# Kernel optimization log

Hardware: AMD Instinct MI355X
Metric: run time of the kernel (lower is better)

Reference implementation:

```python
import jax, jax.numpy as jnp
import numpy as np

INF = 1000000000.0
N_HEAD, QK_DIM, V_DIM, D_MODEL = 16, 64, 64, 1024
B, S = 4, 2048


def rope(x):
    # x: [b, s, h, d]; standard rotary embedding over interleaved pairs
    b, s, h, d = x.shape
    inv_freq = 1.0 / (10000.0 ** (jnp.arange(0, d, 2, dtype=jnp.float32) / d))  # [d/2]
    ang = jnp.arange(s, dtype=jnp.float32)[:, None] * inv_freq  # [s, d/2]
    cos = jnp.cos(ang)[None, :, None, :]  # [1, s, 1, d/2]
    sin = jnp.sin(ang)[None, :, None, :]
    x1, x2 = x[..., 0::2], x[..., 1::2]
    out_even = x1 * cos - x2 * sin
    out_odd = x1 * sin + x2 * cos
    return jnp.stack([out_even, out_odd], axis=-1).reshape(x.shape)


def setup_inputs() -> dict:
    key = jax.random.key(0)
    ks = jax.random.split(key, 8)
    q = jax.random.normal(ks[0], (B, S, D_MODEL), dtype=jnp.float32)
    k = jax.random.normal(ks[1], (B, S, D_MODEL), dtype=jnp.float32)
    v = jax.random.normal(ks[2], (B, S, D_MODEL), dtype=jnp.float32)
    sd = 1.0 / np.sqrt(D_MODEL)
    Wq = jax.random.normal(ks[3], (D_MODEL, N_HEAD * QK_DIM), dtype=jnp.float32) * sd
    Wk = jax.random.normal(ks[4], (D_MODEL, N_HEAD * QK_DIM), dtype=jnp.float32) * sd
    Wv = jax.random.normal(ks[5], (D_MODEL, N_HEAD * V_DIM), dtype=jnp.float32) * sd
    Wo = jax.random.normal(ks[6], (N_HEAD * V_DIM, D_MODEL), dtype=jnp.float32) * (1.0 / np.sqrt(N_HEAD * V_DIM))
    mask = jnp.broadcast_to(jnp.tril(jnp.ones((S, S), dtype=jnp.int32)), (B, S, S))  # causal
    return {"q": q, "k": k, "v": v, "Wq": Wq, "Wk": Wk, "Wv": Wv, "Wo": Wo, "mask": mask}


def reference(q, k, v, Wq, Wk, Wv, Wo, mask):
    b, ql, _ = q.shape
    kl = k.shape[1]
    Q = (q @ Wq).reshape(b, ql, N_HEAD, QK_DIM)
    K = (k @ Wk).reshape(b, kl, N_HEAD, QK_DIM)
    V = (v @ Wv).reshape(b, kl, N_HEAD, V_DIM)
    Q, K = rope(Q), rope(K)
    scale = QK_DIM ** 0.5
    # [b, h, q, k]
    attn = jnp.einsum('bqhd,bkhd->bhqk', Q / scale, K)
    attn = jnp.where(mask[:, None, :, :] == 0, -INF, attn)
    attn = jax.nn.softmax(attn, axis=-1)
    out = jnp.einsum('bhqk,bkhd->bqhd', attn, V).reshape(b, ql, N_HEAD * V_DIM)
    return out @ Wo
```

## Files before the change

### kernel.cpp

```cpp
#include <hip/hip_runtime.h>
#include <hip/hip_bf16.h>


typedef __attribute__((ext_vector_type(8))) short bf16x8;
typedef __attribute__((ext_vector_type(4))) float f32x4;

static __device__ __forceinline__ short f2bf(float f) {
    union { float f; unsigned u; } v; v.f = f;
    unsigned r = v.u + 0x7fffu + ((v.u >> 16) & 1u);
    return (short)(r >> 16);
}
static __device__ __forceinline__ float bf2f(short s) {
    union { unsigned u; float f; } v; v.u = ((unsigned)(unsigned short)s) << 16;
    return v.f;
}

static __device__ __forceinline__ void gload_lds16(const short* g, short* l) {
    __builtin_amdgcn_global_load_lds(
        (const __attribute__((address_space(1))) void*)g,
        (__attribute__((address_space(3))) void*)l, 16, 0, 0);
}

__global__ __launch_bounds__(256) void cvt4_k(const float* __restrict__ in,
                                              short* __restrict__ out, int n4) {
    int i = blockIdx.x * 256 + threadIdx.x;
    if (i < n4) {
        float4 v = ((const float4*)in)[i];
        unsigned lo = (unsigned)(unsigned short)f2bf(v.x) |
                      ((unsigned)(unsigned short)f2bf(v.y) << 16);
        unsigned hi = (unsigned)(unsigned short)f2bf(v.z) |
                      ((unsigned)(unsigned short)f2bf(v.w) << 16);
        uint2 p; p.x = lo; p.y = hi;
        ((uint2*)out)[i] = p;
    }
}

__global__ __launch_bounds__(256) void cvtWT_k(const float* __restrict__ in,
                                               short* __restrict__ out) {
    __shared__ short tile[64][65];
    int n0 = blockIdx.x * 64, k0 = blockIdx.y * 64;
    int t = threadIdx.x;
#pragma unroll
    for (int i = 0; i < 16; ++i) {
        int e = t + i * 256; int r = e >> 6, cq = e & 63;
        tile[r][cq] = f2bf(in[(size_t)(k0 + r) * 1024 + n0 + cq]);
    }
    __syncthreads();
#pragma unroll
    for (int i = 0; i < 16; ++i) {
        int e = t + i * 256; int r = e >> 6, cq = e & 63;
        out[(size_t)(n0 + r) * 1024 + k0 + cq] = tile[cq][r];
    }
}

__global__ __launch_bounds__(256) void gemm128(const short* __restrict__ A,
                                               const short* __restrict__ Wt,
                                               void* __restrict__ outv, int mode) {
    __shared__ __align__(16) short As[128 * 32];
    __shared__ __align__(16) short Bs[128 * 32];
    int t = threadIdx.x, w = t >> 6, lane = t & 63, c = lane & 15, g = lane >> 4;
    int m0 = blockIdx.y * 128, n0 = blockIdx.x * 128;
    int wm = (w >> 1) * 64, wn = (w & 1) * 64;
    f32x4 acc[4][4];
#pragma unroll
    for (int i = 0; i < 4; ++i)
#pragma unroll
        for (int j = 0; j < 4; ++j) acc[i][j] = (f32x4){0.f, 0.f, 0.f, 0.f};
    int srow = w * 32 + (lane >> 2);
    int skc  = (lane & 3) * 8;
    const short* Ag0 = A  + (size_t)(m0 + srow) * 1024 + skc;
    const short* Ag1 = Ag0 + (size_t)16 * 1024;
    const short* Bg0 = Wt + (size_t)(n0 + srow) * 1024 + skc;
    const short* Bg1 = Bg0 + (size_t)16 * 1024;
    short* al0 = &As[(w * 32) * 32];
    short* al1 = &As[(w * 32 + 16) * 32];
    short* bl0 = &Bs[(w * 32) * 32];
    short* bl1 = &Bs[(w * 32 + 16) * 32];
    for (int kt = 0; kt < 1024; kt += 32) {
        __syncthreads();
        gload_lds16(Ag0 + kt, al0);
        gload_lds16(Ag1 + kt, al1);
        gload_lds16(Bg0 + kt, bl0);
        gload_lds16(Bg1 + kt, bl1);
        __syncthreads();
        bf16x8 af[4], bfr[4];
#pragma unroll
        for (int mi = 0; mi < 4; ++mi)
            af[mi] = *(const bf16x8*)&As[(wm + mi * 16 + c) * 32 + g * 8];
#pragma unroll
        for (int ni = 0; ni < 4; ++ni)
            bfr[ni] = *(const bf16x8*)&Bs[(wn + ni * 16 + c) * 32 + g * 8];
#pragma unroll
        for (int mi = 0; mi < 4; ++mi)
#pragma unroll
            for (int ni = 0; ni < 4; ++ni)
                acc[mi][ni] = __builtin_amdgcn_mfma_f32_16x16x32_bf16(
                    af[mi], bfr[ni], acc[mi][ni], 0, 0, 0);
    }
#pragma unroll
    for (int mi = 0; mi < 4; ++mi)
#pragma unroll
        for (int ni = 0; ni < 4; ++ni)
#pragma unroll
            for (int r = 0; r < 4; ++r) {
                int row = m0 + wm + mi * 16 + g * 4 + r;
                int col = n0 + wn + ni * 16 + c;
                float val = acc[mi][ni][r];
                if (mode == 0) {
                    int b = row >> 11, s = row & 2047, h = col >> 6, d = col & 63;
                    ((short*)outv)[(((size_t)b * 16 + h) * 2048 + s) * 64 + d] = f2bf(val);
                } else if (mode == 1) {
                    int b = row >> 11, s = row & 2047, h = col >> 6, d = col & 63;
                    ((short*)outv)[(((size_t)b * 16 + h) * 64 + d) * 2048 + s] = f2bf(val);
                } else {
                    if (!(val == val)) val = 0.f;
                    ((float*)outv)[(size_t)row * 1024 + col] = val;
                }
            }
}

__global__ __launch_bounds__(256) void rope_k(short* __restrict__ buf) {
    int idx = blockIdx.x * 256 + threadIdx.x;
    int j = idx & 31; int s = (idx >> 5) & 2047; int bh = idx >> 16;
    size_t off = ((size_t)bh * 2048 + s) * 64 + 2 * j;
    unsigned pr = *(unsigned*)&buf[off];
    float x1 = bf2f((short)(pr & 0xffff));
    float x2 = bf2f((short)(pr >> 16));
    float inv = expf(-(float)j * (9.210340371976184f / 32.0f));
    float ang = (float)s * inv;
    float sn = sinf(ang), cs = cosf(ang);
    float e = x1 * cs - x2 * sn;
    float o = x1 * sn + x2 * cs;
    unsigned op = (unsigned)(unsigned short)f2bf(e) |
                  ((unsigned)(unsigned short)f2bf(o) << 16);
    *(unsigned*)&buf[off] = op;
}

__global__ __launch_bounds__(256) void attn_k(const short* __restrict__ Qb,
                                              const short* __restrict__ Kb,
                                              const short* __restrict__ Vt,
                                              short* __restrict__ ctx) {
    __shared__ __align__(16) short Kl[64 * 72];
    __shared__ __align__(16) short Vl[64 * 72];
    __shared__ __align__(16) short Pl[4 * 16 * 72];
    int bx = blockIdx.x, bh = blockIdx.y;
    int t = threadIdx.x, w = t >> 6, lane = t & 63, c = lane & 15, g = lane >> 4;
    int b = bh >> 4, h = bh & 15;
    const short* Qp = Qb + (size_t)bh * 2048 * 64;
    const short* Kp = Kb + (size_t)bh * 2048 * 64;
    const short* Vp = Vt + (size_t)bh * 64 * 2048;
    short* Pw = Pl + w * 16 * 72;
    int ch0 = t * 2, ch1 = t * 2 + 1;
    int row0 = ch0 >> 3, cc0 = ch0 & 7, row1 = ch1 >> 3, cc1 = ch1 & 7;
    for (int pass = 0; pass < 2; ++pass) {
        int qblk = pass ? (31 - bx) : bx;
        int q0 = qblk * 64;
        int qrow = q0 + w * 16 + c;
        bf16x8 qa0 = *(const bf16x8*)(Qp + (size_t)qrow * 64 + g * 8);
        bf16x8 qa1 = *(const bf16x8*)(Qp + (size_t)qrow * 64 + 32 + g * 8);
        f32x4 oacc[4];
        float m_i[4], l_i[4];
#pragma unroll
        for (int r = 0; r < 4; ++r) {
            oacc[r] = (f32x4){0.f, 0.f, 0.f, 0.f};
            m_i[r] = -1e30f; l_i[r] = 0.f;
        }
        uint4 kv0 = *(const uint4*)(Kp + (size_t)row0 * 64 + cc0 * 8);
        uint4 kv1 = *(const uint4*)(Kp + (size_t)row1 * 64 + cc1 * 8);
        uint4 vv0 = *(const uint4*)(Vp + (size_t)row0 * 2048 + cc0 * 8);
        uint4 vv1 = *(const uint4*)(Vp + (size_t)row1 * 2048 + cc1 * 8);
        for (int kb = 0; kb <= qblk; ++kb) {
            int k0 = kb * 64;
            __syncthreads();
            *(uint4*)&Kl[row0 * 72 + cc0 * 8] = kv0;
            *(uint4*)&Kl[row1 * 72 + cc1 * 8] = kv1;
            *(uint4*)&Vl[row0 * 72 + cc0 * 8] = vv0;
            *(uint4*)&Vl[row1 * 72 + cc1 * 8] = vv1;
            __syncthreads();
            if (kb < qblk) {
                int kn = k0 + 64;
                kv0 = *(const uint4*)(Kp + (size_t)(kn + row0) * 64 + cc0 * 8);
                kv1 = *(const uint4*)(Kp + (size_t)(kn + row1) * 64 + cc1 * 8);
                vv0 = *(const uint4*)(Vp + (size_t)row0 * 2048 + kn + cc0 * 8);
                vv1 = *(const uint4*)(Vp + (size_t)row1 * 2048 + kn + cc1 * 8);
            }
            f32x4 sacc[4];
#pragma unroll
            for (int ns = 0; ns < 4; ++ns) sacc[ns] = (f32x4){0.f, 0.f, 0.f, 0.f};
#pragma unroll
            for (int ns = 0; ns < 4; ++ns) {
                bf16x8 b0 = *(const bf16x8*)&Kl[(ns * 16 + c) * 72 + g * 8];
                bf16x8 b1 = *(const bf16x8*)&Kl[(ns * 16 + c) * 72 + 32 + g * 8];
                sacc[ns] = __builtin_amdgcn_mfma_f32_16x16x32_bf16(qa0, b0, sacc[ns], 0, 0, 0);
                sacc[ns] = __builtin_amdgcn_mfma_f32_16x16x32_bf16(qa1, b1, sacc[ns], 0, 0, 0);
            }
            float sv[4][4], pr[4][4];
#pragma unroll
            for (int ns = 0; ns < 4; ++ns)
#pragma unroll
                for (int r = 0; r < 4; ++r) {
                    float x = sacc[ns][r] * 0.125f;
                    int qi = q0 + w * 16 + g * 4 + r;
                    int kj = k0 + ns * 16 + c;
                    sv[ns][r] = (kj > qi) ? -1e30f : x;
                }
#pragma unroll
            for (int r = 0; r < 4; ++r) {
                float bm = fmaxf(fmaxf(sv[0][r], sv[1][r]), fmaxf(sv[2][r], sv[3][r]));
#pragma unroll
                for (int off = 1; off < 16; off <<= 1) bm = fmaxf(bm, __shfl_xor(bm, off));
                float mn = fmaxf(m_i[r], bm);
                float alpha = __expf(m_i[r] - mn);
                float rs = 0.f;
#pragma unroll
                for (int ns = 0; ns < 4; ++ns) {
                    float p = __expf(sv[ns][r] - mn);
                    pr[ns][r] = p; rs += p;
                }
#pragma unroll
                for (int off = 1; off < 16; off <<= 1) rs += __shfl_xor(rs, off);
                l_i[r] = l_i[r] * alpha + rs;
                m_i[r] = mn;
#pragma unroll
                for (int vs = 0; vs < 4; ++vs) oacc[vs][r] *= alpha;
            }
#pragma unroll
            for (int ns = 0; ns < 4; ++ns)
#pragma unroll
                for (int r = 0; r < 4; ++r)
                    Pw[(g * 4 + r) * 72 + ns * 16 + c] = f2bf(pr[ns][r]);
#pragma unroll
            for (int ks = 0; ks < 2; ++ks) {
                bf16x8 pa = *(const bf16x8*)&Pw[c * 72 + ks * 32 + g * 8];
#pragma unroll
                for (int vs = 0; vs < 4; ++vs) {
                    bf16x8 bv = *(const bf16x8*)&Vl[(vs * 16 + c) * 72 + ks * 32 + g * 8];
                    oacc[vs] = __builtin_amdgcn_mfma_f32_16x16x32_bf16(pa, bv, oacc[vs], 0, 0, 0);
                }
            }
        }
#pragma unroll
        for (int vs = 0; vs < 4; ++vs)
#pragma unroll
            for (int r = 0; r < 4; ++r) {
                float val = oacc[vs][r] / l_i[r];
                int qi = q0 + w * 16 + g * 4 + r;
                ctx[((size_t)b * 2048 + qi) * 1024 + h * 64 + vs * 16 + c] = f2bf(val);
            }
    }
}

extern "C" void kernel_launch(void* const* d_in, const int* in_sizes, int n_in,
                              void* d_out, int out_size, void* d_ws, size_t ws_size,
                              hipStream_t stream) {
    const float* q  = (const float*)d_in[0];
    const float* k  = (const float*)d_in[1];
    const float* v  = (const float*)d_in[2];
    const float* Wq = (const float*)d_in[3];
    const float* Wk = (const float*)d_in[4];
    const float* Wv = (const float*)d_in[5];
    const float* Wo = (const float*)d_in[6];
    char* sc = (char*)d_in[7];
    const size_t MB = 1024 * 1024;
    short* qb16 = (short*)(sc + 0 * MB);
    short* kb16 = (short*)(sc + 16 * MB);
    short* vb16 = (short*)(sc + 32 * MB);
    short* WqT  = (short*)(sc + 48 * MB);
    short* WkT  = (short*)(sc + 50 * MB);
    short* WvT  = (short*)(sc + 52 * MB);
    short* WoT  = (short*)(sc + 54 * MB);
    short* qbuf = (short*)d_in[0];
    short* kbuf = (short*)d_in[1];
    short* vtb  = (short*)d_in[2];
    short* ctx  = qb16;
    const int NTOK4 = 4 * 2048 * 1024 / 4;

    cvt4_k<<<NTOK4 / 256, 256, 0, stream>>>(q, qb16, NTOK4);
    cvt4_k<<<NTOK4 / 256, 256, 0, stream>>>(k, kb16, NTOK4);
    cvt4_k<<<NTOK4 / 256, 256, 0, stream>>>(v, vb16, NTOK4);
    dim3 tg(16, 16);
    cvtWT_k<<<tg, 256, 0, stream>>>(Wq, WqT);
    cvtWT_k<<<tg, 256, 0, stream>>>(Wk, WkT);
    cvtWT_k<<<tg, 256, 0, stream>>>(Wv, WvT);
    cvtWT_k<<<tg, 256, 0, stream>>>(Wo, WoT);

    dim3 gg(8, 64);
    gemm128<<<gg, 256, 0, stream>>>(qb16, WqT, qbuf, 0);
    gemm128<<<gg, 256, 0, stream>>>(kb16, WkT, kbuf, 0);
    gemm128<<<gg, 256, 0, stream>>>(vb16, WvT, vtb, 1);

    rope_k<<<16384, 256, 0, stream>>>(qbuf);
    rope_k<<<16384, 256, 0, stream>>>(kbuf);

    dim3 ag(16, 64);
    attn_k<<<ag, 256, 0, stream>>>(qbuf, kbuf, vtb, ctx);

    gemm128<<<gg, 256, 0, stream>>>(ctx, WoT, d_out, 2);
}
```

Baseline: 478.5 us.

## Batch launches and streamline attention softmax with lazy rescale and MFMA row sums

Merges the three input conversions, four weight transposes, three QKV GEMMs and two RoPE passes into single launches indexed by grid z/y. This cuts launch overhead and small-grid tail effects. The attention scale and the log2(e) factor are folded into Q during RoPE so the softmax can use exp2f. The causal mask is applied only on the diagonal block, and the running max is rescaled only when it grows by more than a threshold. Row sums are computed by an MFMA against a ones vector instead of shuffles, and s_setprio hints are placed around the MFMA sections.

```diff
diff --git a/kernel.cpp b/kernel.cpp
--- a/kernel.cpp
+++ b/kernel.cpp
@@ -21,23 +21,34 @@
         (__attribute__((address_space(3))) void*)l, 16, 0, 0);
 }
 
-__global__ __launch_bounds__(256) void cvt4_k(const float* __restrict__ in,
+__global__ __launch_bounds__(256) void cvt3_k(const float* __restrict__ q,
+                                              const float* __restrict__ k,
+                                              const float* __restrict__ v,
                                               short* __restrict__ out, int n4) {
+    int z = blockIdx.y;
+    const float* in = (z == 0) ? q : (z == 1) ? k : v;
+    short* o = out + (size_t)z * 8388608;
     int i = blockIdx.x * 256 + threadIdx.x;
     if (i < n4) {
-        float4 v = ((const float4*)in)[i];
-        unsigned lo = (unsigned)(unsigned short)f2bf(v.x) |
-                      ((unsigned)(unsigned short)f2bf(v.y) << 16);
-        unsigned hi = (unsigned)(unsigned short)f2bf(v.z) |
-                      ((unsigned)(unsigned short)f2bf(v.w) << 16);
+        float4 vv = ((const float4*)in)[i];
+        unsigned lo = (unsigned)(unsigned short)f2bf(vv.x) |
+                      ((unsigned)(unsigned short)f2bf(vv.y) << 16);
+        unsigned hi = (unsigned)(unsigned short)f2bf(vv.z) |
+                      ((unsigned)(unsigned short)f2bf(vv.w) << 16);
         uint2 p; p.x = lo; p.y = hi;
-        ((uint2*)out)[i] = p;
-    }
-}
-
-__global__ __launch_bounds__(256) void cvtWT_k(const float* __restrict__ in,
-                                               short* __restrict__ out) {
+        ((uint2*)o)[i] = p;
+    }
+}
+
+__global__ __launch_bounds__(256) void cvtWT4_k(const float* __restrict__ Wq,
+                                                const float* __restrict__ Wk,
+                                                const float* __restrict__ Wv,
+                                                const float* __restrict__ Wo,
+                                                short* __restrict__ outT) {
     __shared__ short tile[64][65];
+    int z = blockIdx.z;
+    const float* in = (z == 0) ? Wq : (z == 1) ? Wk : (z == 2) ? Wv : Wo;
+    short* out = outT + (size_t)z * 1048576;
     int n0 = blockIdx.x * 64, k0 = blockIdx.y * 64;
     int t = threadIdx.x;
 #pragma unroll
@@ -53,9 +64,9 @@
     }
 }
 
-__global__ __launch_bounds__(256) void gemm128(const short* __restrict__ A,
-                                               const short* __restrict__ Wt,
-                                               void* __restrict__ outv, int mode) {
+static __device__ __forceinline__ void gemm_core(const short* __restrict__ A,
+                                                 const short* __restrict__ Wt,
+                                                 void* __restrict__ outv, int mode) {
     __shared__ __align__(16) short As[128 * 32];
     __shared__ __align__(16) short Bs[128 * 32];
     int t = threadIdx.x, w = t >> 6, lane = t & 63, c = lane & 15, g = lane >> 4;
@@ -119,7 +130,29 @@
             }
 }
 
-__global__ __launch_bounds__(256) void rope_k(short* __restrict__ buf) {
+__global__ __launch_bounds__(256) void gemm_qkv_k(const short* __restrict__ Ab,
+                                                  const short* __restrict__ Wtb,
+                                                  void* __restrict__ oq,
+                                                  void* __restrict__ ok,
+                                                  void* __restrict__ ov) {
+    int z = blockIdx.z;
+    const short* A  = Ab  + (size_t)z * 8388608;
+    const short* Wt = Wtb + (size_t)z * 1048576;
+    void* o = (z == 0) ? oq : (z == 1) ? ok : ov;
+    gemm_core(A, Wt, o, (z == 2) ? 1 : 0);
+}
+
+__global__ __launch_bounds__(256) void gemm_o_k(const short* __restrict__ A,
+                                                const short* __restrict__ Wt,
+                                                void* __restrict__ o) {
+    gemm_core(A, Wt, o, 2);
+}
+
+__global__ __launch_bounds__(256) void rope2_k(short* __restrict__ qb,
+                                               short* __restrict__ kb) {
+    int z = blockIdx.y;
+    short* buf = z ? kb : qb;
+    float scale = z ? 1.0f : 0.18033688011112042f;
     int idx = blockIdx.x * 256 + threadIdx.x;
     int j = idx & 31; int s = (idx >> 5) & 2047; int bh = idx >> 16;
     size_t off = ((size_t)bh * 2048 + s) * 64 + 2 * j;
@@ -129,8 +162,8 @@
     float inv = expf(-(float)j * (9.210340371976184f / 32.0f));
     float ang = (float)s * inv;
     float sn = sinf(ang), cs = cosf(ang);
-    float e = x1 * cs - x2 * sn;
-    float o = x1 * sn + x2 * cs;
+    float e = (x1 * cs - x2 * sn) * scale;
+    float o = (x1 * sn + x2 * cs) * scale;
     unsigned op = (unsigned)(unsigned short)f2bf(e) |
                   ((unsigned)(unsigned short)f2bf(o) << 16);
     *(unsigned*)&buf[off] = op;
@@ -152,6 +185,9 @@
     short* Pw = Pl + w * 16 * 72;
     int ch0 = t * 2, ch1 = t * 2 + 1;
     int row0 = ch0 >> 3, cc0 = ch0 & 7, row1 = ch1 >> 3, cc1 = ch1 & 7;
+    bf16x8 ones;
+#pragma unroll
+    for (int i = 0; i < 8; ++i) ones[i] = (short)0x3F80;
     for (int pass = 0; pass < 2; ++pass) {
         int qblk = pass ? (31 - bx) : bx;
         int q0 = qblk * 64;
@@ -187,6 +223,7 @@
             f32x4 sacc[4];
 #pragma unroll
             for (int ns = 0; ns < 4; ++ns) sacc[ns] = (f32x4){0.f, 0.f, 0.f, 0.f};
+            __builtin_amdgcn_s_setprio(1);
 #pragma unroll
             for (int ns = 0; ns < 4; ++ns) {
                 bf16x8 b0 = *(const bf16x8*)&Kl[(ns * 16 + c) * 72 + g * 8];
@@ -194,50 +231,55 @@
                 sacc[ns] = __builtin_amdgcn_mfma_f32_16x16x32_bf16(qa0, b0, sacc[ns], 0, 0, 0);
                 sacc[ns] = __builtin_amdgcn_mfma_f32_16x16x32_bf16(qa1, b1, sacc[ns], 0, 0, 0);
             }
-            float sv[4][4], pr[4][4];
+            __builtin_amdgcn_s_setprio(0);
+            float sv[4][4];
 #pragma unroll
             for (int ns = 0; ns < 4; ++ns)
 #pragma unroll
+                for (int r = 0; r < 4; ++r) sv[ns][r] = sacc[ns][r];
+            if (kb == qblk) {
+#pragma unroll
                 for (int r = 0; r < 4; ++r) {
-                    float x = sacc[ns][r] * 0.125f;
                     int qi = q0 + w * 16 + g * 4 + r;
-                    int kj = k0 + ns * 16 + c;
-                    sv[ns][r] = (kj > qi) ? -1e30f : x;
+#pragma unroll
+                    for (int ns = 0; ns < 4; ++ns) {
+                        int kj = k0 + ns * 16 + c;
+                        if (kj > qi) sv[ns][r] = -1e30f;
+                    }
                 }
+            }
 #pragma unroll
             for (int r = 0; r < 4; ++r) {
                 float bm = fmaxf(fmaxf(sv[0][r], sv[1][r]), fmaxf(sv[2][r], sv[3][r]));
 #pragma unroll
                 for (int off = 1; off < 16; off <<= 1) bm = fmaxf(bm, __shfl_xor(bm, off));
-                float mn = fmaxf(m_i[r], bm);
-                float alpha = __expf(m_i[r] - mn);
-                float rs = 0.f;
-#pragma unroll
-                for (int ns = 0; ns < 4; ++ns) {
-                    float p = __expf(sv[ns][r] - mn);
-                    pr[ns][r] = p; rs += p;
+                if (!__all(bm <= m_i[r] + 8.f)) {
+                    float mn = fmaxf(m_i[r], bm);
+                    float alpha = exp2f(m_i[r] - mn);
+#pragma unroll
+                    for (int vs = 0; vs < 4; ++vs) oacc[vs][r] *= alpha;
+                    l_i[r] *= alpha;
+                    m_i[r] = mn;
                 }
 #pragma unroll
-                for (int off = 1; off < 16; off <<= 1) rs += __shfl_xor(rs, off);
-                l_i[r] = l_i[r] * alpha + rs;
-                m_i[r] = mn;
-#pragma unroll
-                for (int vs = 0; vs < 4; ++vs) oacc[vs][r] *= alpha;
-            }
-#pragma unroll
-            for (int ns = 0; ns < 4; ++ns)
-#pragma unroll
-                for (int r = 0; r < 4; ++r)
-                    Pw[(g * 4 + r) * 72 + ns * 16 + c] = f2bf(pr[ns][r]);
+                for (int ns = 0; ns < 4; ++ns)
+                    Pw[(g * 4 + r) * 72 + ns * 16 + c] = f2bf(exp2f(sv[ns][r] - m_i[r]));
+            }
+            f32x4 sumacc = (f32x4){0.f, 0.f, 0.f, 0.f};
+            __builtin_amdgcn_s_setprio(1);
 #pragma unroll
             for (int ks = 0; ks < 2; ++ks) {
                 bf16x8 pa = *(const bf16x8*)&Pw[c * 72 + ks * 32 + g * 8];
+                sumacc = __builtin_amdgcn_mfma_f32_16x16x32_bf16(pa, ones, sumacc, 0, 0, 0);
 #pragma unroll
                 for (int vs = 0; vs < 4; ++vs) {
                     bf16x8 bv = *(const bf16x8*)&Vl[(vs * 16 + c) * 72 + ks * 32 + g * 8];
                     oacc[vs] = __builtin_amdgcn_mfma_f32_16x16x32_bf16(pa, bv, oacc[vs], 0, 0, 0);
                 }
             }
+            __builtin_amdgcn_s_setprio(0);
+#pragma unroll
+            for (int r = 0; r < 4; ++r) l_i[r] += sumacc[r];
         }
 #pragma unroll
         for (int vs = 0; vs < 4; ++vs)
@@ -263,11 +305,7 @@
     char* sc = (char*)d_in[7];
     const size_t MB = 1024 * 1024;
     short* qb16 = (short*)(sc + 0 * MB);
-    short* kb16 = (short*)(sc + 16 * MB);
-    short* vb16 = (short*)(sc + 32 * MB);
     short* WqT  = (short*)(sc + 48 * MB);
-    short* WkT  = (short*)(sc + 50 * MB);
-    short* WvT  = (short*)(sc + 52 * MB);
     short* WoT  = (short*)(sc + 54 * MB);
     short* qbuf = (short*)d_in[0];
     short* kbuf = (short*)d_in[1];
@@ -275,25 +313,10 @@
     short* ctx  = qb16;
     const int NTOK4 = 4 * 2048 * 1024 / 4;
 
-    cvt4_k<<<NTOK4 / 256, 256, 0, stream>>>(q, qb16, NTOK4);
-    cvt4_k<<<NTOK4 / 256, 256, 0, stream>>>(k, kb16, NTOK4);
-    cvt4_k<<<NTOK4 / 256, 256, 0, stream>>>(v, vb16, NTOK4);
-    dim3 tg(16, 16);
-    cvtWT_k<<<tg, 256, 0, stream>>>(Wq, WqT);
-    cvtWT_k<<<tg, 256, 0, stream>>>(Wk, WkT);
-    cvtWT_k<<<tg, 256, 0, stream>>>(Wv, WvT);
-    cvtWT_k<<<tg, 256, 0, stream>>>(Wo, WoT);
-
-    dim3 gg(8, 64);
-    gemm128<<<gg, 256, 0, stream>>>(qb16, WqT, qbuf, 0);
-    gemm128<<<gg, 256, 0, stream>>>(kb16, WkT, kbuf, 0);
-    gemm128<<<gg, 256, 0, stream>>>(vb16, WvT, vtb, 1);
-
-    rope_k<<<16384, 256, 0, stream>>>(qbuf);
-    rope_k<<<16384, 256, 0, stream>>>(kbuf);
-
-    dim3 ag(16, 64);
-    attn_k<<<ag, 256, 0, stream>>>(qbuf, kbuf, vtb, ctx);
-
-    gemm128<<<gg, 256, 0, stream>>>(ctx, WoT, d_out, 2);
-}
+    cvt3_k<<<dim3(NTOK4 / 256, 3), 256, 0, stream>>>(q, k, v, qb16, NTOK4);
+    cvtWT4_k<<<dim3(16, 16, 4), 256, 0, stream>>>(Wq, Wk, Wv, Wo, WqT);
+    gemm_qkv_k<<<dim3(8, 64, 3), 256, 0, stream>>>(qb16, WqT, qbuf, kbuf, vtb);
+    rope2_k<<<dim3(16384, 2), 256, 0, stream>>>(qbuf, kbuf);
+    attn_k<<<dim3(16, 64), 256, 0, stream>>>(qbuf, kbuf, vtb, ctx);
+    gemm_o_k<<<dim3(8, 64), 256, 0, stream>>>(ctx, WoT, d_out);
+}
```

After: 458.2 us. -4.2%, faster.
